# Kernel optimization log

Hardware: AMD Instinct MI355X
Metric: run time of the kernel (lower is better)

Reference implementation:

```python
import jax, jax.numpy as jnp
import numpy as np
import math

B, T, C, H = 4, 1024, 1024, 16
D = C // H  # head dim = 64

def setup_inputs() -> dict:
    key = jax.random.key(0)
    ks = jax.random.split(key, 10)
    s = 1.0 / math.sqrt(C)
    x = jax.random.normal(ks[0], (B, T, C), dtype=jnp.float32)
    pad = (jax.random.uniform(ks[1], (B, T)) < 0.2).astype(jnp.float32)
    # ensure first token of every row is unpadded so softmax rows are well-posed
    pad = pad.at[:, 0].set(0.0)
    Wq = jax.random.normal(ks[2], (C, C), dtype=jnp.float32) * s
    bq = jnp.zeros((C,), dtype=jnp.float32)
    Wk = jax.random.normal(ks[3], (C, C), dtype=jnp.float32) * s
    bk = jnp.zeros((C,), dtype=jnp.float32)
    Wv = jax.random.normal(ks[4], (C, C), dtype=jnp.float32) * s
    bv = jnp.zeros((C,), dtype=jnp.float32)
    Wp = jax.random.normal(ks[5], (C, C), dtype=jnp.float32) * s
    bp = jnp.zeros((C,), dtype=jnp.float32)
    return {"x": x, "x_padding_judge": pad, "Wq": Wq, "bq": bq,
            "Wk": Wk, "bk": bk, "Wv": Wv, "bv": bv, "Wp": Wp, "bp": bp}

def reference(x, x_padding_judge, Wq, bq, Wk, bk, Wv, bv, Wp, bp):
    # keep flag: 1.0 where token is real, 0.0 where padded
    keep = 1.0 - x_padding_judge                      # [B, T]
    mask = keep[:, :, None] * keep[:, None, :]        # [B, T, T] outer product
    # projections, split heads: [B, H, T, D]
    def heads(w, b):
        return (x @ w + b).reshape(B, T, H, D).transpose(0, 2, 1, 3)
    q, k, v = heads(Wq, bq), heads(Wk, bk), heads(Wv, bv)
    att = jnp.einsum('bhqd,bhkd->bhqk', q, k) * (1.0 / math.sqrt(D))
    # attn_pdrop=0 => att_full is all ones; masked_fill where mask == 0
    att = jnp.where(mask[:, None, :, :] == 0, -1e9, att)
    att = jax.nn.softmax(att, axis=-1)
    y = jnp.einsum('bhqk,bhkd->bhqd', att, v)         # [B, H, T, D]
    y = y.transpose(0, 2, 1, 3).reshape(B, T, C)
    return y @ Wp + bp
```

## Files before the change

### kernel.cpp

```cpp
#include <hip/hip_runtime.h>
#include <hip/hip_bf16.h>
#include <math.h>

#define Bb 4
#define Tt 1024
#define Cc 1024
#define Hh 16
#define Dd 64

typedef __attribute__((ext_vector_type(8))) _Float16 half8;
typedef __attribute__((ext_vector_type(4))) _Float16 half4;
typedef __attribute__((ext_vector_type(4))) float floatx4;


struct PrepP { const float* x; _Float16* xh; const float* W[4]; _Float16* out[4]; };

__global__ __launch_bounds__(256) void prep_all(PrepP p)
{
    if (blockIdx.x < 256) {
        const int m16 = blockIdx.x;
        const int r   = threadIdx.x & 15;
        const int kc0 = threadIdx.x >> 4;
        const float* src = p.x + (size_t)(m16 * 16 + r) * 1024;
        _Float16*   dst = p.xh + (size_t)m16 * 16384 + r * 8;
#pragma unroll
        for (int c8 = 0; c8 < 8; ++c8) {
            const int kc = kc0 + c8 * 16;
            float4 a = *(const float4*)(src + kc * 8);
            float4 b = *(const float4*)(src + kc * 8 + 4);
            half8 h;
            h[0] = (_Float16)a.x; h[1] = (_Float16)a.y; h[2] = (_Float16)a.z; h[3] = (_Float16)a.w;
            h[4] = (_Float16)b.x; h[5] = (_Float16)b.y; h[6] = (_Float16)b.z; h[7] = (_Float16)b.w;
            *(half8*)(dst + kc * 128) = h;
        }
        return;
    }
    const int bid2 = blockIdx.x - 256;
    const int z    = bid2 >> 8;
    const int rem  = bid2 & 255;
    const int n0   = (rem & 15) * 64;
    const int k0   = (rem >> 4) * 64;
    const float* __restrict__ W = p.W[z];
    _Float16* __restrict__ outp = p.out[z];
    __shared__ float tile[64][65];
    const int tr  = threadIdx.x >> 4;
    const int tc4 = (threadIdx.x & 15) * 4;

#pragma unroll
    for (int i = 0; i < 4; ++i) {
        const int kk = tr + i * 16;
        float4 v = *(const float4*)(W + (size_t)(k0 + kk) * 1024 + n0 + tc4);
        tile[kk][tc4 + 0] = v.x;
        tile[kk][tc4 + 1] = v.y;
        tile[kk][tc4 + 2] = v.z;
        tile[kk][tc4 + 3] = v.w;
    }
    __syncthreads();
#pragma unroll
    for (int i = 0; i < 4; ++i) {
        half4 h;
#pragma unroll
        for (int c = 0; c < 4; ++c) h[c] = (_Float16)tile[tc4 + c][tr + i * 16];
        _Float16* dst = outp + (size_t)((n0 >> 4) + i) * 16384
                        + ((k0 + tc4) >> 3) * 128 + tr * 8 + (tc4 & 7);
        *(half4*)dst = h;
    }
}

struct QkvP { const _Float16* Wt[3]; const float* bias[3];
              _Float16* qb; _Float16* kb; _Float16* vt; };

__global__ __launch_bounds__(256) void gemm_qkv(const _Float16* __restrict__ xh, QkvP p)
{
    const int z = blockIdx.z;
    const _Float16* __restrict__ Wt   = p.Wt[z];
    const float* __restrict__    bias = p.bias[z];

    const int tid  = threadIdx.x;
    const int lane = tid & 63;
    const int w    = tid >> 6;
    const int wr   = w >> 1, wc = w & 1;
    const int quad = lane >> 4;
    const int l15  = lane & 15;
    const int bm   = blockIdx.x * 128;
    const int bn   = blockIdx.y * 128;

    const _Float16* Ap[4];
    const _Float16* Bp[4];
#pragma unroll
    for (int i = 0; i < 4; ++i)
        Ap[i] = xh + (size_t)((bm >> 4) + wr * 4 + i) * 16384 + lane * 8;
#pragma unroll
    for (int j = 0; j < 4; ++j)
        Bp[j] = Wt + (size_t)((bn >> 4) + wc * 4 + j) * 16384 + lane * 8;

    floatx4 acc[4][4];
#pragma unroll
    for (int i = 0; i < 4; ++i)
#pragma unroll
        for (int j = 0; j < 4; ++j)
            acc[i][j] = (floatx4){0.f, 0.f, 0.f, 0.f};

    half8 a0[4], b0[4];
#pragma unroll
    for (int i = 0; i < 4; ++i) a0[i] = *(const half8*)(Ap[i]);
#pragma unroll
    for (int j = 0; j < 4; ++j) b0[j] = *(const half8*)(Bp[j]);

    for (int kt = 0; kt < 1024; kt += 64) {
        half8 a1[4], b1[4];
        const size_t o1 = (size_t)(kt + 32) * 16;
#pragma unroll
        for (int i = 0; i < 4; ++i) a1[i] = *(const half8*)(Ap[i] + o1);
#pragma unroll
        for (int j = 0; j < 4; ++j) b1[j] = *(const half8*)(Bp[j] + o1);
#pragma unroll
        for (int i = 0; i < 4; ++i)
#pragma unroll
            for (int j = 0; j < 4; ++j)
                acc[i][j] = __builtin_amdgcn_mfma_f32_16x16x32_f16(a0[i], b0[j], acc[i][j], 0, 0, 0);

        const size_t o2 = (kt + 64 < 1024) ? (size_t)(kt + 64) * 16 : 0;
#pragma unroll
        for (int i = 0; i < 4; ++i) a0[i] = *(const half8*)(Ap[i] + o2);
#pragma unroll
        for (int j = 0; j < 4; ++j) b0[j] = *(const half8*)(Bp[j] + o2);
#pragma unroll
        for (int i = 0; i < 4; ++i)
#pragma unroll
            for (int j = 0; j < 4; ++j)
                acc[i][j] = __builtin_amdgcn_mfma_f32_16x16x32_f16(a1[i], b1[j], acc[i][j], 0, 0, 0);
    }

    if (z == 2) {
#pragma unroll
        for (int j = 0; j < 4; ++j) {
            const int col = bn + wc * 64 + j * 16 + l15;
            const int h  = col >> 6;
            const float bj = bias[col];
#pragma unroll
            for (int i = 0; i < 4; ++i) {
                const int t0 = bm + wr * 64 + i * 16 + quad * 4;
                const int bh = (t0 >> 10) * 16 + h;
                const int tm = t0 & 1023;
                half4 pk;
#pragma unroll
                for (int r = 0; r < 4; ++r) pk[r] = (_Float16)(acc[i][j][r] + bj);
                *(half4*)(p.vt + (size_t)bh * 65536 + (size_t)j * 16384
                          + (tm >> 3) * 128 + l15 * 8 + (tm & 7)) = pk;
            }
        }
    } else {
        _Float16* outp = (z == 0) ? p.qb : p.kb;
#pragma unroll
        for (int j = 0; j < 4; ++j) {
            const int col = bn + wc * 64 + j * 16 + l15;
            const int h  = col >> 6;
            const int dd = col & 63;
            const float bj = bias[col];
            const int doff = (dd >> 3) * 128 + (dd & 7);
#pragma unroll
            for (int i = 0; i < 4; ++i) {
#pragma unroll
                for (int r = 0; r < 4; ++r) {
                    const int tg = bm + wr * 64 + i * 16 + quad * 4 + r;
                    const int bh = (tg >> 10) * 16 + h;
                    const int tm = tg & 1023;
                    outp[(size_t)bh * 65536 + (tm >> 4) * 1024 + doff + (tm & 15) * 8] =
                        (_Float16)(acc[i][j][r] + bj);
                }
            }
        }
    }
}

__global__ __launch_bounds__(256) void attn_mfma(
    const _Float16* __restrict__ qb, const _Float16* __restrict__ kb,
    const _Float16* __restrict__ vt, const float* __restrict__ padj,
    _Float16* __restrict__ yh)
{
    __shared__ __align__(16) _Float16 Ps[4][2048];

    const int tid  = threadIdx.x;
    const int lane = tid & 63;
    const int w    = tid >> 6;
    const int quad = lane >> 4;
    const int l15  = lane & 15;
    const int bh   = blockIdx.x;
    const int q0   = blockIdx.y * 128;
    const int b    = bh >> 4;
    const int h    = bh & 15;

    const _Float16* qf = qb + (size_t)bh * 65536;
    const _Float16* kf = kb + (size_t)bh * 65536;
    const _Float16* vf = vt + (size_t)bh * 65536;
    const float*    pk_row = padj + b * Tt;

    half8 bq[2][2];
#pragma unroll
    for (int ks = 0; ks < 2; ++ks)
#pragma unroll
        for (int nq = 0; nq < 2; ++nq)
            bq[ks][nq] = *(const half8*)(qf + (size_t)((q0 >> 4) + w * 2 + nq) * 1024
                                         + ks * 512 + lane * 8);
    float kq[2];
#pragma unroll
    for (int nq = 0; nq < 2; ++nq)
        kq[nq] = 1.0f - pk_row[q0 + w * 32 + nq * 16 + l15];

    floatx4 O[2][4];
    floatx4 l_acc[2];
#pragma unroll
    for (int mi = 0; mi < 2; ++mi) {
#pragma unroll
        for (int dj = 0; dj < 4; ++dj) O[mi][dj] = (floatx4){0.f, 0.f, 0.f, 0.f};
        l_acc[mi] = (floatx4){0.f, 0.f, 0.f, 0.f};
    }
    half8 ones;
#pragma unroll
    for (int j = 0; j < 8; ++j) ones[j] = (_Float16)1.0f;

    constexpr float SC = 0.18033688011112042f;

    for (int kt = 0; kt < Tt; kt += 64) {
        half8 ak[2][4], bv[2][4];
#pragma unroll
        for (int ks = 0; ks < 2; ++ks)
#pragma unroll
            for (int mk = 0; mk < 4; ++mk)
                ak[ks][mk] = *(const half8*)(kf + (size_t)((kt >> 4) + mk) * 1024
                                             + ks * 512 + lane * 8);
#pragma unroll
        for (int ks = 0; ks < 2; ++ks)
#pragma unroll
            for (int dj = 0; dj < 4; ++dj)
                bv[ks][dj] = *(const half8*)(vf + (size_t)dj * 16384 + (kt >> 3) * 128
                                             + ks * 512 + lane * 8);
        float4 kk4[4];
#pragma unroll
        for (int mk = 0; mk < 4; ++mk)
            kk4[mk] = *(const float4*)(pk_row + kt + mk * 16 + quad * 4);

        floatx4 ST[4][2];
#pragma unroll
        for (int mk = 0; mk < 4; ++mk)
#pragma unroll
            for (int nq = 0; nq < 2; ++nq)
                ST[mk][nq] = (floatx4){0.f, 0.f, 0.f, 0.f};
#pragma unroll
        for (int ks = 0; ks < 2; ++ks)
#pragma unroll
            for (int mk = 0; mk < 4; ++mk)
#pragma unroll
                for (int nq = 0; nq < 2; ++nq)
                    ST[mk][nq] = __builtin_amdgcn_mfma_f32_16x16x32_f16(
                        ak[ks][mk], bq[ks][nq], ST[mk][nq], 0, 0, 0);

#pragma unroll
        for (int mk = 0; mk < 4; ++mk) {
            const float kkr[4] = {1.0f - kk4[mk].x, 1.0f - kk4[mk].y,
                                  1.0f - kk4[mk].z, 1.0f - kk4[mk].w};
#pragma unroll
            for (int nq = 0; nq < 2; ++nq) {
                half4 pk;
#pragma unroll
                for (int r = 0; r < 4; ++r) {
                    const float e = __builtin_amdgcn_exp2f(ST[mk][nq][r] * SC);
                    const float pv = (kq[nq] == 0.0f) ? 1.0f : kkr[r] * e;
                    pk[r] = (_Float16)pv;
                }
                *(half4*)&Ps[w][((mk * 2 + (quad >> 1)) * 32 + nq * 16 + l15) * 8
                               + (quad & 1) * 4] = pk;
            }
        }

#pragma unroll
        for (int ks = 0; ks < 2; ++ks) {
            half8 ap[2];
#pragma unroll
            for (int mi = 0; mi < 2; ++mi)
                ap[mi] = *(const half8*)&Ps[w][((ks * 4 + quad) * 32 + mi * 16 + l15) * 8];
#pragma unroll
            for (int mi = 0; mi < 2; ++mi) {
#pragma unroll
                for (int dj = 0; dj < 4; ++dj)
                    O[mi][dj] = __builtin_amdgcn_mfma_f32_16x16x32_f16(
                        ap[mi], bv[ks][dj], O[mi][dj], 0, 0, 0);
                l_acc[mi] = __builtin_amdgcn_mfma_f32_16x16x32_f16(
                    ap[mi], ones, l_acc[mi], 0, 0, 0);
            }
        }
    }

#pragma unroll
    for (int mi = 0; mi < 2; ++mi) {
#pragma unroll
        for (int r = 0; r < 4; ++r) {
            const int rowl  = w * 32 + mi * 16 + quad * 4 + r;
            const int token = b * Tt + q0 + rowl;
            const float inv = 1.0f / l_acc[mi][r];
            const size_t tb = (size_t)(token >> 4) * 16384 + (token & 15) * 8;
#pragma unroll
            for (int dj = 0; dj < 4; ++dj) {
                const int col = h * 64 + dj * 16 + l15;
                yh[tb + (col >> 3) * 128 + (col & 7)] = (_Float16)(O[mi][dj][r] * inv);
            }
        }
    }
}

__global__ __launch_bounds__(256) void gemm_proj(const _Float16* __restrict__ Ay,
                                                 const _Float16* __restrict__ Bt,
                                                 const float* __restrict__ bias,
                                                 float* __restrict__ out)
{
    const int tid  = threadIdx.x;
    const int lane = tid & 63;
    const int w    = tid >> 6;
    const int quad = lane >> 4;
    const int l15  = lane & 15;
    const int bm   = blockIdx.x * 128;
    const int bn   = blockIdx.y * 64;

    const _Float16* Ap[2];
    const _Float16* Bp[4];
#pragma unroll
    for (int i = 0; i < 2; ++i)
        Ap[i] = Ay + (size_t)((bm >> 4) + w * 2 + i) * 16384 + lane * 8;
#pragma unroll
    for (int j = 0; j < 4; ++j)
        Bp[j] = Bt + (size_t)((bn >> 4) + j) * 16384 + lane * 8;

    floatx4 acc[2][4];
#pragma unroll
    for (int i = 0; i < 2; ++i)
#pragma unroll
        for (int j = 0; j < 4; ++j)
            acc[i][j] = (floatx4){0.f, 0.f, 0.f, 0.f};

    half8 a0[2], b0[4];
#pragma unroll
    for (int i = 0; i < 2; ++i) a0[i] = *(const half8*)(Ap[i]);
#pragma unroll
    for (int j = 0; j < 4; ++j) b0[j] = *(const half8*)(Bp[j]);

    for (int kt = 0; kt < 1024; kt += 64) {
        half8 a1[2], b1[4];
        const size_t o1 = (size_t)(kt + 32) * 16;
#pragma unroll
        for (int i = 0; i < 2; ++i) a1[i] = *(const half8*)(Ap[i] + o1);
#pragma unroll
        for (int j = 0; j < 4; ++j) b1[j] = *(const half8*)(Bp[j] + o1);
#pragma unroll
        for (int i = 0; i < 2; ++i)
#pragma unroll
            for (int j = 0; j < 4; ++j)
                acc[i][j] = __builtin_amdgcn_mfma_f32_16x16x32_f16(a0[i], b0[j], acc[i][j], 0, 0, 0);

        const size_t o2 = (kt + 64 < 1024) ? (size_t)(kt + 64) * 16 : 0;
#pragma unroll
        for (int i = 0; i < 2; ++i) a0[i] = *(const half8*)(Ap[i] + o2);
#pragma unroll
        for (int j = 0; j < 4; ++j) b0[j] = *(const half8*)(Bp[j] + o2);
#pragma unroll
        for (int i = 0; i < 2; ++i)
#pragma unroll
            for (int j = 0; j < 4; ++j)
                acc[i][j] = __builtin_amdgcn_mfma_f32_16x16x32_f16(a1[i], b1[j], acc[i][j], 0, 0, 0);
    }

#pragma unroll
    for (int j = 0; j < 4; ++j) {
        const int col = bn + j * 16 + l15;
        const float bj = bias[col];
#pragma unroll
        for (int i = 0; i < 2; ++i) {
            const int row = bm + w * 32 + i * 16 + quad * 4;
            float* o = out + (size_t)row * 1024 + col;
#pragma unroll
            for (int r = 0; r < 4; ++r)
                o[(size_t)r * 1024] = acc[i][j][r] + bj;
        }
    }
}

extern "C" void kernel_launch(void* const* d_in, const int* in_sizes, int n_in,
                              void* d_out, int out_size, void* d_ws, size_t ws_size,
                              hipStream_t stream)
{
    const float* x    = (const float*)d_in[0];
    const float* padj = (const float*)d_in[1];
    const float* Wq   = (const float*)d_in[2];
    const float* bq   = (const float*)d_in[3];
    const float* Wk   = (const float*)d_in[4];
    const float* bk   = (const float*)d_in[5];
    const float* Wv   = (const float*)d_in[6];
    const float* bv   = (const float*)d_in[7];
    const float* Wp   = (const float*)d_in[8];
    const float* bp   = (const float*)d_in[9];
    float* out = (float*)d_out;

    const size_t MB = 1024 * 1024;
    char* ws = (char*)d_ws;
    _Float16* xh  = (_Float16*)(ws);
    _Float16* Wt0 = (_Float16*)(ws +  8 * MB);
    _Float16* Wt1 = (_Float16*)(ws + 10 * MB);
    _Float16* Wt2 = (_Float16*)(ws + 12 * MB);
    _Float16* Wtp = (_Float16*)(ws + 14 * MB);
    _Float16* qb  = (_Float16*)(ws + 16 * MB);
    _Float16* kb  = (_Float16*)(ws + 24 * MB);
    _Float16* vtb = (_Float16*)(ws + 32 * MB);
    _Float16* yh  = (_Float16*)(ws + 40 * MB);

    PrepP pp;
    pp.x = x; pp.xh = xh;
    pp.W[0] = Wq; pp.W[1] = Wk; pp.W[2] = Wv; pp.W[3] = Wp;
    pp.out[0] = Wt0; pp.out[1] = Wt1; pp.out[2] = Wt2; pp.out[3] = Wtp;
    prep_all<<<1280, 256, 0, stream>>>(pp);

    QkvP qp;
    qp.Wt[0] = Wt0; qp.Wt[1] = Wt1; qp.Wt[2] = Wt2;
    qp.bias[0] = bq; qp.bias[1] = bk; qp.bias[2] = bv;
    qp.qb = qb; qp.kb = kb; qp.vt = vtb;
    gemm_qkv<<<dim3(32, 8, 3), 256, 0, stream>>>(xh, qp);

    attn_mfma<<<dim3(64, 8), 256, 0, stream>>>(qb, kb, vtb, padj, yh);

    gemm_proj<<<dim3(32, 16), 256, 0, stream>>>(yh, Wtp, bp, out);
}
```

Baseline: 186.5 us.

## Stage QKV GEMM tiles through LDS with direct global-to-LDS loads

The QKV projection GEMM previously had each wave load its own A and B fragments straight from global memory into registers, so tiles shared between waves were fetched twice. It now loads each 128x64 A/B k-tile once per block into shared memory using global_load_lds. The waves then read their fragments from LDS between two barriers. This halves global traffic per block, but it drops the previous register double-buffering, so load latency is exposed at every k-step behind a __syncthreads.

```diff
diff --git a/kernel.cpp b/kernel.cpp
--- a/kernel.cpp
+++ b/kernel.cpp
@@ -12,6 +12,13 @@
 typedef __attribute__((ext_vector_type(4))) _Float16 half4;
 typedef __attribute__((ext_vector_type(4))) float floatx4;
 
+
+__device__ __forceinline__ void gload_lds16(const _Float16* g, const _Float16* l)
+{
+    __builtin_amdgcn_global_load_lds(
+        (const __attribute__((address_space(1))) void*)g,
+        (__attribute__((address_space(3))) void*)l, 16, 0, 0);
+}
 
 struct PrepP { const float* x; _Float16* xh; const float* W[4]; _Float16* out[4]; };
 
@@ -85,14 +92,17 @@
     const int bm   = blockIdx.x * 128;
     const int bn   = blockIdx.y * 128;
 
-    const _Float16* Ap[4];
-    const _Float16* Bp[4];
-#pragma unroll
-    for (int i = 0; i < 4; ++i)
-        Ap[i] = xh + (size_t)((bm >> 4) + wr * 4 + i) * 16384 + lane * 8;
-#pragma unroll
-    for (int j = 0; j < 4; ++j)
-        Bp[j] = Wt + (size_t)((bn >> 4) + wc * 4 + j) * 16384 + lane * 8;
+    __shared__ __align__(16) _Float16 As[16][512];
+    __shared__ __align__(16) _Float16 Bs[16][512];
+
+    const _Float16* ga[4];
+    const _Float16* gb[4];
+#pragma unroll
+    for (int c = 0; c < 4; ++c) {
+        const int fa = w * 4 + c;
+        ga[c] = xh + (size_t)((bm >> 4) + (fa >> 1)) * 16384 + (fa & 1) * 512 + lane * 8;
+        gb[c] = Wt + (size_t)((bn >> 4) + (fa >> 1)) * 16384 + (fa & 1) * 512 + lane * 8;
+    }
 
     floatx4 acc[4][4];
 #pragma unroll
@@ -101,35 +111,33 @@
         for (int j = 0; j < 4; ++j)
             acc[i][j] = (floatx4){0.f, 0.f, 0.f, 0.f};
 
-    half8 a0[4], b0[4];
-#pragma unroll
-    for (int i = 0; i < 4; ++i) a0[i] = *(const half8*)(Ap[i]);
-#pragma unroll
-    for (int j = 0; j < 4; ++j) b0[j] = *(const half8*)(Bp[j]);
-
     for (int kt = 0; kt < 1024; kt += 64) {
-        half8 a1[4], b1[4];
-        const size_t o1 = (size_t)(kt + 32) * 16;
-#pragma unroll
-        for (int i = 0; i < 4; ++i) a1[i] = *(const half8*)(Ap[i] + o1);
-#pragma unroll
-        for (int j = 0; j < 4; ++j) b1[j] = *(const half8*)(Bp[j] + o1);
-#pragma unroll
-        for (int i = 0; i < 4; ++i)
+        const size_t ko = (size_t)kt * 16;
+#pragma unroll
+        for (int c = 0; c < 4; ++c)
+            gload_lds16(ga[c] + ko, &As[w * 4 + c][0]);
+#pragma unroll
+        for (int c = 0; c < 4; ++c)
+            gload_lds16(gb[c] + ko, &Bs[w * 4 + c][0]);
+        __syncthreads();
+
+#pragma unroll
+        for (int ks = 0; ks < 2; ++ks) {
+            half8 af[4], bf[4];
+#pragma unroll
+            for (int i = 0; i < 4; ++i)
+                af[i] = *(const half8*)&As[(wr * 4 + i) * 2 + ks][lane * 8];
 #pragma unroll
             for (int j = 0; j < 4; ++j)
-                acc[i][j] = __builtin_amdgcn_mfma_f32_16x16x32_f16(a0[i], b0[j], acc[i][j], 0, 0, 0);
-
-        const size_t o2 = (kt + 64 < 1024) ? (size_t)(kt + 64) * 16 : 0;
-#pragma unroll
-        for (int i = 0; i < 4; ++i) a0[i] = *(const half8*)(Ap[i] + o2);
-#pragma unroll
-        for (int j = 0; j < 4; ++j) b0[j] = *(const half8*)(Bp[j] + o2);
-#pragma unroll
-        for (int i = 0; i < 4; ++i)
-#pragma unroll
-            for (int j = 0; j < 4; ++j)
-                acc[i][j] = __builtin_amdgcn_mfma_f32_16x16x32_f16(a1[i], b1[j], acc[i][j], 0, 0, 0);
+                bf[j] = *(const half8*)&Bs[(wc * 4 + j) * 2 + ks][lane * 8];
+#pragma unroll
+            for (int i = 0; i < 4; ++i)
+#pragma unroll
+                for (int j = 0; j < 4; ++j)
+                    acc[i][j] = __builtin_amdgcn_mfma_f32_16x16x32_f16(
+                        af[i], bf[j], acc[i][j], 0, 0, 0);
+        }
+        __syncthreads();
     }
 
     if (z == 2) {
```

Result: no change. 183.7 us (-1.5%).
